# Kernel tuning notes

Measured on AMD Instinct MI355X. Metric: run time of the kernel, lower is better.

## Reference

```python
import jax, jax.numpy as jnp
import numpy as np

D_MODEL = 1024
H = 16
D_K = D_MODEL // H
B = 2
S = 2048


def setup_inputs() -> dict:
    key = jax.random.key(0)
    ks = jax.random.split(key, 13)
    scale = 1.0 / np.sqrt(D_MODEL)
    inp = {
        "Q": jax.random.normal(ks[0], (B, S, D_MODEL), jnp.float32),
        "K": jax.random.normal(ks[1], (B, S, D_MODEL), jnp.float32),
        "V": jax.random.normal(ks[2], (B, S, D_MODEL), jnp.float32),
        "mask": jax.random.randint(ks[3], (B, 1, S, S), 0, 2, jnp.int32),
        "WQ_w": jax.random.normal(ks[4], (D_MODEL, D_MODEL), jnp.float32) * scale,
        "WQ_b": jax.random.normal(ks[5], (D_MODEL,), jnp.float32) * scale,
        "WK_w": jax.random.normal(ks[6], (D_MODEL, D_MODEL), jnp.float32) * scale,
        "WK_b": jax.random.normal(ks[7], (D_MODEL,), jnp.float32) * scale,
        "WV_w": jax.random.normal(ks[8], (D_MODEL, D_MODEL), jnp.float32) * scale,
        "WV_b": jax.random.normal(ks[9], (D_MODEL,), jnp.float32) * scale,
        "WO_w": jax.random.normal(ks[10], (D_MODEL, D_MODEL), jnp.float32) * scale,
        "WO_b": jax.random.normal(ks[11], (D_MODEL,), jnp.float32) * scale,
    }
    return inp


def _split_heads(x):
    # [B,S,D] -> [B,H,S,d_k]
    b, s, _ = x.shape
    return x.reshape(b, s, H, D_K).transpose(0, 2, 1, 3)


def reference(Q, K, V, mask, WQ_w, WQ_b, WK_w, WK_b, WV_w, WV_b, WO_w, WO_b):
    q = _split_heads(Q @ WQ_w.T + WQ_b)
    k = _split_heads(K @ WK_w.T + WK_b)
    v = _split_heads(V @ WV_w.T + WV_b)
    scores = jnp.einsum("bhqd,bhkd->bhqk", q, k) / jnp.sqrt(jnp.float32(D_K))
    # NOTE: original code fills masked positions with 1e-9 (not -inf) -- replicate faithfully
    scores = jnp.where(mask == 0, jnp.float32(1e-9), scores)
    attn = jax.nn.softmax(scores, axis=-1)
    out = jnp.einsum("bhqk,bhkd->bhqd", attn, v)  # [B,H,S,d_k]
    out = out.transpose(0, 2, 1, 3).reshape(Q.shape[0], -1, D_MODEL)
    return out @ WO_w.T + WO_b
```

## Files before the change

kernel.cpp:

```cpp
#include <hip/hip_runtime.h>
#include <stdint.h>

#define D_MODEL 1024
#define NH 16
#define DKK 64
#define SEQ 2048
#define QSCALE 0.18033688011112042f

using half8 = __attribute__((ext_vector_type(8))) _Float16;
using half4 = __attribute__((ext_vector_type(4))) _Float16;
using half2v = __attribute__((ext_vector_type(2))) _Float16;
using fp16x2 = __attribute__((ext_vector_type(2))) __fp16;
using f32x4 = __attribute__((ext_vector_type(4))) float;

__device__ __forceinline__ f32x4 fz4() { f32x4 v = {0.f, 0.f, 0.f, 0.f}; return v; }

__device__ __forceinline__ void gload16(const void* g, void* l) {
    __builtin_amdgcn_global_load_lds(
        (const __attribute__((address_space(1))) unsigned int*)g,
        (__attribute__((address_space(3))) unsigned int*)l, 16, 0, 0);
}

__device__ __forceinline__ half2v pk2(float a, float b) {
    fp16x2 t = __builtin_amdgcn_cvt_pkrtz(a, b);
    return __builtin_bit_cast(half2v, t);
}

__device__ __forceinline__ half4 pk4(float a, float b, float c, float d) {
    half2v lo = pk2(a, b);
    half2v hi = pk2(c, d);
    half4 r; r.x = lo.x; r.y = lo.y; r.z = hi.x; r.w = hi.y;
    return r;
}

__device__ __forceinline__ int xswz(int bid, int n) {
    return (bid & 7) * (n >> 3) + (bid >> 3);
}

__global__ __launch_bounds__(256) void conv_all(const float* __restrict__ wq,
                                                const float* __restrict__ wk,
                                                const float* __restrict__ wv,
                                                const float* __restrict__ wo,
                                                const float* __restrict__ Q,
                                                const float* __restrict__ K,
                                                const float* __restrict__ V,
                                                _Float16* __restrict__ out) {
    int idx = blockIdx.x * 256 + threadIdx.x;
#pragma unroll
    for (int k = 0; k < 8; ++k) {
        int c = idx + k * 524288;
        const float* src;
        int off;
        if (c < 1048576) {
            int w = c >> 18;
            src = (w == 0) ? wq : (w == 1) ? wk : (w == 2) ? wv : wo;
            off = c & 0x3ffff;
        } else {
            int j = (c >> 20) - 1;
            src = (j == 0) ? Q : (j == 1) ? K : V;
            off = c & 0xfffff;
        }
        float4 v = ((const float4*)src)[off];
        ((half4*)out)[c] = pk4(v.x, v.y, v.z, v.w);
    }
}

__global__ __launch_bounds__(256) void pack_mask_k(const int* __restrict__ mask,
                                                   unsigned int* __restrict__ mbits) {
    int wid = threadIdx.x >> 6, lane = threadIdx.x & 63;
    int row = blockIdx.x * 4 + wid;
    const int* mrow = mask + (size_t)row * SEQ;
    unsigned int* orow = mbits + (size_t)row * (SEQ / 32);
    for (int it = 0; it < SEQ / 64; ++it) {
        int v = mrow[it * 64 + lane];
        unsigned long long bal = __ballot(v != 0);
        if (lane == 0)       orow[it * 2]     = (unsigned int)(bal & 0xffffffffull);
        else if (lane == 32) orow[it * 2 + 1] = (unsigned int)(bal >> 32);
    }
}

__device__ __forceinline__ void gemm_body(const _Float16* __restrict__ A,
                                          const _Float16* __restrict__ Wh,
                                          const float* __restrict__ bias,
                                          void* __restrict__ outp, int omode, float scale) {
    __shared__ __align__(16) _Float16 Asm[2][64 * 64];
    __shared__ __align__(16) _Float16 Bsm[2][128 * 64];
    const int tid = threadIdx.x;
    const int wg = xswz(blockIdx.x, 512);
    const int bm = wg >> 3, bn = wg & 7;
    const int wid = tid >> 6, lane = tid & 63;
    const int li = lane & 15, g = lane >> 4;
    const int wm = wid >> 1, wn = wid & 1;

    const int brow = wid * 32 + (lane >> 3);
    const char* bsrc = (const char*)(Wh + (size_t)(bn * 128 + brow) * D_MODEL)
                       + (((lane & 7) ^ (brow & 7)) * 16);
    const int bdst = wid * 32 * 128;
    const int arow = wid * 16 + (lane >> 3);
    const char* asrc = (const char*)(A + (size_t)(bm * 64 + arow) * D_MODEL)
                       + (((lane & 7) ^ (arow & 7)) * 16);
    const int adst = wid * 16 * 128;

    f32x4 acc[2][4];
#pragma unroll
    for (int i = 0; i < 2; ++i)
#pragma unroll
        for (int j = 0; j < 4; ++j) acc[i][j] = fz4();

    const int o0 = ((g << 4))      ^ ((li & 7) << 4);
    const int o1 = (64 + (g << 4)) ^ ((li & 7) << 4);
    const int abase = wm * 4096 + li * 128;
    const int bbase = wn * 8192 + li * 128;

    auto stage = [&](int it, int buf) {
        const char* bs = bsrc + it * 128;
        char* bd = (char*)&Bsm[buf][0] + bdst;
        gload16(bs,             bd);
        gload16(bs +  8 * 2048, bd + 1024);
        gload16(bs + 16 * 2048, bd + 2048);
        gload16(bs + 24 * 2048, bd + 3072);
        const char* as = asrc + it * 128;
        char* ad = (char*)&Asm[buf][0] + adst;
        gload16(as,            ad);
        gload16(as + 8 * 2048, ad + 1024);
    };

    stage(0, 0);
    __syncthreads();

    for (int it = 0; it < 16; ++it) {
        const int cur = it & 1;
        if (it + 1 < 16) stage(it + 1, cur ^ 1);
        const char* ab = (const char*)&Asm[cur][0];
        const char* bb = (const char*)&Bsm[cur][0];
#pragma unroll
        for (int s = 0; s < 2; ++s) {
            const int oS = s ? o1 : o0;
            half8 af0 = *(const half8*)(ab + abase + 0    + oS);
            half8 af1 = *(const half8*)(ab + abase + 2048 + oS);
            half8 bf[4];
#pragma unroll
            for (int nt = 0; nt < 4; ++nt)
                bf[nt] = *(const half8*)(bb + bbase + nt * 2048 + oS);
#pragma unroll
            for (int nt = 0; nt < 4; ++nt) {
                acc[0][nt] = __builtin_amdgcn_mfma_f32_16x16x32_f16(af0, bf[nt], acc[0][nt], 0, 0, 0);
                acc[1][nt] = __builtin_amdgcn_mfma_f32_16x16x32_f16(af1, bf[nt], acc[1][nt], 0, 0, 0);
            }
        }
        __syncthreads();
    }

#pragma unroll
    for (int nt = 0; nt < 4; ++nt) {
        int n = bn * 128 + wn * 64 + nt * 16 + li;
        float bv = bias[n];
#pragma unroll
        for (int mt = 0; mt < 2; ++mt) {
            if (omode == 1) {
                int s0 = bm * 64 + wm * 32 + mt * 16 + g * 4;
                int b = (bm * 64) >> 11;
                int h = n >> 6, d = n & 63;
                half4 hv = pk4(acc[mt][nt][0] + bv, acc[mt][nt][1] + bv,
                               acc[mt][nt][2] + bv, acc[mt][nt][3] + bv);
                *(half4*)((_Float16*)outp +
                          ((((size_t)(b * NH + h)) * DKK + d) * SEQ + (s0 & (SEQ - 1)))) = hv;
            } else {
#pragma unroll
                for (int r = 0; r < 4; ++r) {
                    int m = bm * 64 + wm * 32 + mt * 16 + g * 4 + r;
                    float val = (acc[mt][nt][r] + bv) * scale;
                    if (omode == 2) {
                        ((float*)outp)[(size_t)m * D_MODEL + n] = val;
                    } else {
                        int b = m >> 11, s = m & (SEQ - 1);
                        int h = n >> 6, d = n & 63;
                        ((_Float16*)outp)[(((size_t)(b * NH + h)) * SEQ + s) * DKK + d] =
                            (_Float16)val;
                    }
                }
            }
        }
    }
}

struct QkvArgs {
    const float *b0, *b1, *b2;
    _Float16 *o0, *o1, *o2;
};

__global__ __launch_bounds__(256) void gemm_qkv(const _Float16* __restrict__ Ah,
                                                const _Float16* __restrict__ cw,
                                                QkvArgs ga) {
    const int z = blockIdx.y;
    const _Float16* A  = Ah + (size_t)z * (D_MODEL * 4096);
    const float* bi = (z == 0) ? ga.b0 : (z == 1) ? ga.b1 : ga.b2;
    _Float16*    o  = (z == 0) ? ga.o0 : (z == 1) ? ga.o1 : ga.o2;
    gemm_body(A, cw + (size_t)z * D_MODEL * D_MODEL, bi, o,
              (z == 2) ? 1 : 0, (z == 0) ? QSCALE : 1.0f);
}

__global__ __launch_bounds__(256) void gemm_out(const _Float16* __restrict__ A,
                                                const _Float16* __restrict__ cw,
                                                const float* __restrict__ bias,
                                                float* __restrict__ out) {
    gemm_body(A, cw, bias, out, 2, 1.0f);
}

__global__ __launch_bounds__(256) void attn_fwd(const _Float16* __restrict__ q,
                                                const _Float16* __restrict__ kk,
                                                const _Float16* __restrict__ vt,
                                                const unsigned int* __restrict__ mb,
                                                _Float16* __restrict__ aout) {
    __shared__ __align__(16) _Float16 klds[2][64 * 64];
    __shared__ __align__(16) _Float16 vlds[2][64 * 64];
    __shared__ __align__(16) _Float16 plds[4][32 * 72];
    const int wg = xswz(blockIdx.x, 512);
    const int qblk = wg & 15, bh = wg >> 4;
    const int b = bh >> 4, h = bh & 15;
    const int tid = threadIdx.x, wid = tid >> 6, lane = tid & 63;
    const int li = lane & 15, g = lane >> 4;
    const _Float16* qp = q  + (size_t)bh * SEQ * DKK;
    const _Float16* kp = kk + (size_t)bh * SEQ * DKK;
    const _Float16* vp = vt + (size_t)bh * DKK * SEQ;
    const int qrow0 = qblk * 128 + wid * 32;

    half8 qf[2][2];
#pragma unroll
    for (int qh = 0; qh < 2; ++qh)
#pragma unroll
        for (int s = 0; s < 2; ++s)
            qf[qh][s] = *(const half8*)(qp + (size_t)(qrow0 + qh * 16 + li) * DKK + s * 32 + g * 8);

    const int srow = wid * 16 + (lane >> 3);
    const int sswz = ((lane & 7) ^ (srow & 7)) * 16;
    const char* ksrc = (const char*)(kp + (size_t)srow * DKK) + sswz;
    const char* vsrc = (const char*)(vp + (size_t)srow * SEQ) + sswz;
    const int sdst = wid * 2048;

    auto stage = [&](int it, int buf) {
        const char* ks = ksrc + (size_t)it * 8192;
        const char* vs = vsrc + (size_t)it * 128;
        char* kd = (char*)&klds[buf][0] + sdst;
        char* vd = (char*)&vlds[buf][0] + sdst;
        gload16(ks,                       kd);
        gload16(ks + 8 * 128,             kd + 1024);
        gload16(vs,                       vd);
        gload16(vs + 8 * (size_t)SEQ * 2, vd + 1024);
    };

    f32x4 O[2][4];
#pragma unroll
    for (int qh = 0; qh < 2; ++qh)
#pragma unroll
        for (int dt = 0; dt < 4; ++dt) O[qh][dt] = fz4();
    float lsum[2] = {0.f, 0.f};

    const unsigned int* m0 = mb + ((size_t)b * SEQ + qrow0 + li) * (SEQ / 32);
    const unsigned int* m1 = m0 + (size_t)16 * (SEQ / 32);

    char* pw = (char*)&plds[wid][0];
    const int pwo = li * 144 + g * 8;
    const int pro = li * 144 + g * 16;

    const int o0 = ((g << 4))      ^ ((li & 7) << 4);
    const int o1 = (64 + (g << 4)) ^ ((li & 7) << 4);
    const int kfb = li * 128;

    stage(0, 0);
    __syncthreads();

    for (int it = 0; it < SEQ / 64; ++it) {
        const int cur = it & 1;
        if (it + 1 < SEQ / 64) stage(it + 1, cur ^ 1);
        uint2 ma  = *(const uint2*)(m0 + it * 2);
        uint2 mbw = *(const uint2*)(m1 + it * 2);

        f32x4 st[2][4];
#pragma unroll
        for (int qh = 0; qh < 2; ++qh)
#pragma unroll
            for (int t = 0; t < 4; ++t) st[qh][t] = fz4();
        const char* kb_ = (const char*)&klds[cur][0];
        __builtin_amdgcn_s_setprio(1);
#pragma unroll
        for (int t = 0; t < 4; ++t) {
            half8 kf0 = *(const half8*)(kb_ + kfb + t * 2048 + o0);
            half8 kf1 = *(const half8*)(kb_ + kfb + t * 2048 + o1);
            st[0][t] = __builtin_amdgcn_mfma_f32_16x16x32_f16(kf0, qf[0][0], st[0][t], 0, 0, 0);
            st[0][t] = __builtin_amdgcn_mfma_f32_16x16x32_f16(kf1, qf[0][1], st[0][t], 0, 0, 0);
            st[1][t] = __builtin_amdgcn_mfma_f32_16x16x32_f16(kf0, qf[1][0], st[1][t], 0, 0, 0);
            st[1][t] = __builtin_amdgcn_mfma_f32_16x16x32_f16(kf1, qf[1][1], st[1][t], 0, 0, 0);
        }
        __builtin_amdgcn_s_setprio(0);

#pragma unroll
        for (int qh = 0; qh < 2; ++qh) {
            unsigned wlo = (qh ? mbw.x : ma.x) >> (g * 4);
            unsigned whi = (qh ? mbw.y : ma.y) >> (g * 4);
#pragma unroll
            for (int t = 0; t < 4; ++t) {
                unsigned wsel = (t < 2) ? wlo : whi;
                const int sh = (t & 1) << 4;
                float e0 = __builtin_amdgcn_exp2f(st[qh][t][0]);
                float e1 = __builtin_amdgcn_exp2f(st[qh][t][1]);
                float e2 = __builtin_amdgcn_exp2f(st[qh][t][2]);
                float e3 = __builtin_amdgcn_exp2f(st[qh][t][3]);
                float p0 = ((wsel >> (sh + 0)) & 1u) ? e0 : 1.0f;
                float p1 = ((wsel >> (sh + 1)) & 1u) ? e1 : 1.0f;
                float p2 = ((wsel >> (sh + 2)) & 1u) ? e2 : 1.0f;
                float p3 = ((wsel >> (sh + 3)) & 1u) ? e3 : 1.0f;
                lsum[qh] += (p0 + p1) + (p2 + p3);
                *(half4*)(pw + pwo + qh * 2304 + t * 32) = pk4(p0, p1, p2, p3);
            }
        }

        half8 pB[2][2];
#pragma unroll
        for (int qh = 0; qh < 2; ++qh)
#pragma unroll
            for (int s = 0; s < 2; ++s)
                pB[qh][s] = *(const half8*)(pw + pro + qh * 2304 + s * 64);
        const char* vb_ = (const char*)&vlds[cur][0];
        __builtin_amdgcn_s_setprio(1);
#pragma unroll
        for (int dt = 0; dt < 4; ++dt) {
            half8 vf0 = *(const half8*)(vb_ + kfb + dt * 2048 + o0);
            half8 vf1 = *(const half8*)(vb_ + kfb + dt * 2048 + o1);
            O[0][dt] = __builtin_amdgcn_mfma_f32_16x16x32_f16(vf0, pB[0][0], O[0][dt], 0, 0, 0);
            O[0][dt] = __builtin_amdgcn_mfma_f32_16x16x32_f16(vf1, pB[0][1], O[0][dt], 0, 0, 0);
            O[1][dt] = __builtin_amdgcn_mfma_f32_16x16x32_f16(vf0, pB[1][0], O[1][dt], 0, 0, 0);
            O[1][dt] = __builtin_amdgcn_mfma_f32_16x16x32_f16(vf1, pB[1][1], O[1][dt], 0, 0, 0);
        }
        __builtin_amdgcn_s_setprio(0);
        __syncthreads();
    }

#pragma unroll
    for (int qh = 0; qh < 2; ++qh) {
        float ssum = lsum[qh];
        ssum += __shfl_xor(ssum, 16);
        ssum += __shfl_xor(ssum, 32);
        float inv = 1.0f / ssum;
        _Float16* orow = aout + ((size_t)(b * SEQ + qrow0 + qh * 16 + li)) * D_MODEL
                         + h * DKK + g * 4;
#pragma unroll
        for (int dt = 0; dt < 4; ++dt)
            *(half4*)(orow + dt * 16) = pk4(O[qh][dt][0] * inv, O[qh][dt][1] * inv,
                                            O[qh][dt][2] * inv, O[qh][dt][3] * inv);
    }
}

extern "C" void kernel_launch(void* const* d_in, const int* in_sizes, int n_in,
                              void* d_out, int out_size, void* d_ws, size_t ws_size,
                              hipStream_t stream) {
    const float* Q    = (const float*)d_in[0];
    const float* Kin  = (const float*)d_in[1];
    const float* Vin  = (const float*)d_in[2];
    const int*   mask = (const int*)d_in[3];
    const float* WQw = (const float*)d_in[4];
    const float* WQb = (const float*)d_in[5];
    const float* WKw = (const float*)d_in[6];
    const float* WKb = (const float*)d_in[7];
    const float* WVw = (const float*)d_in[8];
    const float* WVb = (const float*)d_in[9];
    const float* WOw = (const float*)d_in[10];
    const float* WOb = (const float*)d_in[11];

    char* w = (char*)d_ws;
    const size_t MB = 1ull << 20;
    _Float16* cw  = (_Float16*)(w);
    _Float16* Ah  = (_Float16*)(w + 8 * MB);
    _Float16* ab  = (_Float16*)(w + 8 * MB);
    _Float16* qb  = (_Float16*)(w + 32 * MB);
    _Float16* kbf = (_Float16*)(w + 40 * MB);
    _Float16* vtb = (_Float16*)(w + 48 * MB);
    unsigned int* mbits = (unsigned int*)(w + 56 * MB);

    conv_all<<<dim3(2048), dim3(256), 0, stream>>>(WQw, WKw, WVw, WOw, Q, Kin, Vin, cw);
    pack_mask_k<<<dim3(1024), dim3(256), 0, stream>>>(mask, mbits);

    QkvArgs ga;
    ga.b0 = WQb; ga.b1 = WKb; ga.b2 = WVb;
    ga.o0 = qb;  ga.o1 = kbf; ga.o2 = vtb;
    gemm_qkv<<<dim3(512, 3), dim3(256), 0, stream>>>(Ah, cw, ga);

    attn_fwd<<<dim3(512), dim3(256), 0, stream>>>(qb, kbf, vtb, mbits, ab);

    gemm_out<<<dim3(512), dim3(256), 0, stream>>>(ab, cw + 3ull * D_MODEL * D_MODEL, WOb,
                                                  (float*)d_out);
}
```

Baseline: 147.7 us.

## Halve attention query tile per wave and compute row sums via MFMA

```diff
diff --git a/kernel.cpp b/kernel.cpp
--- a/kernel.cpp
+++ b/kernel.cpp
@@ -207,30 +207,32 @@
     gemm_body(A, cw, bias, out, 2, 1.0f);
 }
 
-__global__ __launch_bounds__(256) void attn_fwd(const _Float16* __restrict__ q,
-                                                const _Float16* __restrict__ kk,
-                                                const _Float16* __restrict__ vt,
-                                                const unsigned int* __restrict__ mb,
-                                                _Float16* __restrict__ aout) {
+__global__ __launch_bounds__(256, 4) void attn_fwd(const _Float16* __restrict__ q,
+                                                   const _Float16* __restrict__ kk,
+                                                   const _Float16* __restrict__ vt,
+                                                   const unsigned int* __restrict__ mb,
+                                                   _Float16* __restrict__ aout) {
     __shared__ __align__(16) _Float16 klds[2][64 * 64];
     __shared__ __align__(16) _Float16 vlds[2][64 * 64];
-    __shared__ __align__(16) _Float16 plds[4][32 * 72];
-    const int wg = xswz(blockIdx.x, 512);
-    const int qblk = wg & 15, bh = wg >> 4;
+    __shared__ __align__(16) _Float16 plds[4][16 * 64];
+    const int wg = xswz(blockIdx.x, 1024);
+    const int qblk = wg & 31, bh = wg >> 5;
     const int b = bh >> 4, h = bh & 15;
     const int tid = threadIdx.x, wid = tid >> 6, lane = tid & 63;
     const int li = lane & 15, g = lane >> 4;
     const _Float16* qp = q  + (size_t)bh * SEQ * DKK;
     const _Float16* kp = kk + (size_t)bh * SEQ * DKK;
     const _Float16* vp = vt + (size_t)bh * DKK * SEQ;
-    const int qrow0 = qblk * 128 + wid * 32;
-
-    half8 qf[2][2];
-#pragma unroll
-    for (int qh = 0; qh < 2; ++qh)
-#pragma unroll
-        for (int s = 0; s < 2; ++s)
-            qf[qh][s] = *(const half8*)(qp + (size_t)(qrow0 + qh * 16 + li) * DKK + s * 32 + g * 8);
+    const int qrow0 = qblk * 64 + wid * 16;
+
+    half8 qf[2];
+#pragma unroll
+    for (int s = 0; s < 2; ++s)
+        qf[s] = *(const half8*)(qp + (size_t)(qrow0 + li) * DKK + s * 32 + g * 8);
+
+    half8 ones;
+#pragma unroll
+    for (int j = 0; j < 8; ++j) ones[j] = (_Float16)1.0f;
 
     const int srow = wid * 16 + (lane >> 3);
     const int sswz = ((lane & 7) ^ (srow & 7)) * 16;
@@ -249,19 +251,16 @@
         gload16(vs + 8 * (size_t)SEQ * 2, vd + 1024);
     };
 
-    f32x4 O[2][4];
-#pragma unroll
-    for (int qh = 0; qh < 2; ++qh)
-#pragma unroll
-        for (int dt = 0; dt < 4; ++dt) O[qh][dt] = fz4();
-    float lsum[2] = {0.f, 0.f};
+    f32x4 O[4];
+#pragma unroll
+    for (int dt = 0; dt < 4; ++dt) O[dt] = fz4();
+    f32x4 Ol = fz4();
 
     const unsigned int* m0 = mb + ((size_t)b * SEQ + qrow0 + li) * (SEQ / 32);
-    const unsigned int* m1 = m0 + (size_t)16 * (SEQ / 32);
 
     char* pw = (char*)&plds[wid][0];
-    const int pwo = li * 144 + g * 8;
-    const int pro = li * 144 + g * 16;
+    const int pswz = (li & 7) << 4;
+    const int prow = li * 128;
 
     const int o0 = ((g << 4))      ^ ((li & 7) << 4);
     const int o1 = (64 + (g << 4)) ^ ((li & 7) << 4);
@@ -273,82 +272,62 @@
     for (int it = 0; it < SEQ / 64; ++it) {
         const int cur = it & 1;
         if (it + 1 < SEQ / 64) stage(it + 1, cur ^ 1);
-        uint2 ma  = *(const uint2*)(m0 + it * 2);
-        uint2 mbw = *(const uint2*)(m1 + it * 2);
-
-        f32x4 st[2][4];
-#pragma unroll
-        for (int qh = 0; qh < 2; ++qh)
-#pragma unroll
-            for (int t = 0; t < 4; ++t) st[qh][t] = fz4();
+        uint2 ma = *(const uint2*)(m0 + it * 2);
+
+        f32x4 st[4];
+#pragma unroll
+        for (int t = 0; t < 4; ++t) st[t] = fz4();
         const char* kb_ = (const char*)&klds[cur][0];
         __builtin_amdgcn_s_setprio(1);
 #pragma unroll
         for (int t = 0; t < 4; ++t) {
             half8 kf0 = *(const half8*)(kb_ + kfb + t * 2048 + o0);
             half8 kf1 = *(const half8*)(kb_ + kfb + t * 2048 + o1);
-            st[0][t] = __builtin_amdgcn_mfma_f32_16x16x32_f16(kf0, qf[0][0], st[0][t], 0, 0, 0);
-            st[0][t] = __builtin_amdgcn_mfma_f32_16x16x32_f16(kf1, qf[0][1], st[0][t], 0, 0, 0);
-            st[1][t] = __builtin_amdgcn_mfma_f32_16x16x32_f16(kf0, qf[1][0], st[1][t], 0, 0, 0);
-            st[1][t] = __builtin_amdgcn_mfma_f32_16x16x32_f16(kf1, qf[1][1], st[1][t], 0, 0, 0);
+            st[t] = __builtin_amdgcn_mfma_f32_16x16x32_f16(kf0, qf[0], st[t], 0, 0, 0);
+            st[t] = __builtin_amdgcn_mfma_f32_16x16x32_f16(kf1, qf[1], st[t], 0, 0, 0);
         }
         __builtin_amdgcn_s_setprio(0);
 
 #pragma unroll
-        for (int qh = 0; qh < 2; ++qh) {
-            unsigned wlo = (qh ? mbw.x : ma.x) >> (g * 4);
-            unsigned whi = (qh ? mbw.y : ma.y) >> (g * 4);
-#pragma unroll
-            for (int t = 0; t < 4; ++t) {
-                unsigned wsel = (t < 2) ? wlo : whi;
-                const int sh = (t & 1) << 4;
-                float e0 = __builtin_amdgcn_exp2f(st[qh][t][0]);
-                float e1 = __builtin_amdgcn_exp2f(st[qh][t][1]);
-                float e2 = __builtin_amdgcn_exp2f(st[qh][t][2]);
-                float e3 = __builtin_amdgcn_exp2f(st[qh][t][3]);
-                float p0 = ((wsel >> (sh + 0)) & 1u) ? e0 : 1.0f;
-                float p1 = ((wsel >> (sh + 1)) & 1u) ? e1 : 1.0f;
-                float p2 = ((wsel >> (sh + 2)) & 1u) ? e2 : 1.0f;
-                float p3 = ((wsel >> (sh + 3)) & 1u) ? e3 : 1.0f;
-                lsum[qh] += (p0 + p1) + (p2 + p3);
-                *(half4*)(pw + pwo + qh * 2304 + t * 32) = pk4(p0, p1, p2, p3);
-            }
-        }
-
-        half8 pB[2][2];
-#pragma unroll
-        for (int qh = 0; qh < 2; ++qh)
-#pragma unroll
-            for (int s = 0; s < 2; ++s)
-                pB[qh][s] = *(const half8*)(pw + pro + qh * 2304 + s * 64);
+        for (int t = 0; t < 4; ++t) {
+            unsigned wsel = ((t < 2) ? ma.x : ma.y) >> (g * 4);
+            const int sh = (t & 1) << 4;
+            float e0 = __builtin_amdgcn_exp2f(st[t][0]);
+            float e1 = __builtin_amdgcn_exp2f(st[t][1]);
+            float e2 = __builtin_amdgcn_exp2f(st[t][2]);
+            float e3 = __builtin_amdgcn_exp2f(st[t][3]);
+            float p0 = ((wsel >> (sh + 0)) & 1u) ? e0 : 1.0f;
+            float p1 = ((wsel >> (sh + 1)) & 1u) ? e1 : 1.0f;
+            float p2 = ((wsel >> (sh + 2)) & 1u) ? e2 : 1.0f;
+            float p3 = ((wsel >> (sh + 3)) & 1u) ? e3 : 1.0f;
+            *(half4*)(pw + prow + ((t * 32 + g * 8) ^ pswz)) = pk4(p0, p1, p2, p3);
+        }
+
+        half8 pB[2];
+#pragma unroll
+        for (int s = 0; s < 2; ++s)
+            pB[s] = *(const half8*)(pw + prow + ((s * 64 + g * 16) ^ pswz));
         const char* vb_ = (const char*)&vlds[cur][0];
         __builtin_amdgcn_s_setprio(1);
+        Ol = __builtin_amdgcn_mfma_f32_16x16x32_f16(ones, pB[0], Ol, 0, 0, 0);
+        Ol = __builtin_amdgcn_mfma_f32_16x16x32_f16(ones, pB[1], Ol, 0, 0, 0);
 #pragma unroll
         for (int dt = 0; dt < 4; ++dt) {
             half8 vf0 = *(const half8*)(vb_ + kfb + dt * 2048 + o0);
             half8 vf1 = *(const half8*)(vb_ + kfb + dt * 2048 + o1);
-            O[0][dt] = __builtin_amdgcn_mfma_f32_16x16x32_f16(vf0, pB[0][0], O[0][dt], 0, 0, 0);
-            O[0][dt] = __builtin_amdgcn_mfma_f32_16x16x32_f16(vf1, pB[0][1], O[0][dt], 0, 0, 0);
-            O[1][dt] = __builtin_amdgcn_mfma_f32_16x16x32_f16(vf0, pB[1][0], O[1][dt], 0, 0, 0);
-            O[1][dt] = __builtin_amdgcn_mfma_f32_16x16x32_f16(vf1, pB[1][1], O[1][dt], 0, 0, 0);
+            O[dt] = __builtin_amdgcn_mfma_f32_16x16x32_f16(vf0, pB[0], O[dt], 0, 0, 0);
+            O[dt] = __builtin_amdgcn_mfma_f32_16x16x32_f16(vf1, pB[1], O[dt], 0, 0, 0);
         }
         __builtin_amdgcn_s_setprio(0);
         __syncthreads();
     }
 
-#pragma unroll
-    for (int qh = 0; qh < 2; ++qh) {
-        float ssum = lsum[qh];
-        ssum += __shfl_xor(ssum, 16);
-        ssum += __shfl_xor(ssum, 32);
-        float inv = 1.0f / ssum;
-        _Float16* orow = aout + ((size_t)(b * SEQ + qrow0 + qh * 16 + li)) * D_MODEL
-                         + h * DKK + g * 4;
-#pragma unroll
-        for (int dt = 0; dt < 4; ++dt)
-            *(half4*)(orow + dt * 16) = pk4(O[qh][dt][0] * inv, O[qh][dt][1] * inv,
-                                            O[qh][dt][2] * inv, O[qh][dt][3] * inv);
-    }
+    float inv = 1.0f / Ol[0];
+    _Float16* orow = aout + ((size_t)(b * SEQ + qrow0 + li)) * D_MODEL + h * DKK + g * 4;
+#pragma unroll
+    for (int dt = 0; dt < 4; ++dt)
+        *(half4*)(orow + dt * 16) = pk4(O[dt][0] * inv, O[dt][1] * inv,
+                                        O[dt][2] * inv, O[dt][3] * inv);
 }
 
 extern "C" void kernel_launch(void* const* d_in, const int* in_sizes, int n_in,
@@ -385,7 +364,7 @@
     ga.o0 = qb;  ga.o1 = kbf; ga.o2 = vtb;
     gemm_qkv<<<dim3(512, 3), dim3(256), 0, stream>>>(Ah, cw, ga);
 
-    attn_fwd<<<dim3(512), dim3(256), 0, stream>>>(qb, kbf, vtb, mbits, ab);
+    attn_fwd<<<dim3(1024), dim3(256), 0, stream>>>(qb, kbf, vtb, mbits, ab);
 
     gemm_out<<<dim3(512), dim3(256), 0, stream>>>(ab, cw + 3ull * D_MODEL * D_MODEL, WOb,
                                                   (float*)d_out);
```

Result: faster. 144.4 us (-2.2%).
